# Kernel optimization log

Hardware: AMD Instinct MI355X
Metric: run time of the kernel (lower is better)

The kernel has to match this reference:

```python
import jax, jax.numpy as jnp
import numpy as np

B, T, C = 2, 512, 2048      # batch, seq_len, n_embd (= dim_att)
H, Dh = 32, 64              # num_heads, head_size
D_MIX, D_DECAY = 32, 64     # LoRA ranks (n_embd < 4096)
LAYER_ID, N_LAYER = 12, 24
LN_EPS = 1e-5


def setup_inputs() -> dict:
    key = jax.random.key(0)
    ks = jax.random.split(key, 18)
    s = 1.0 / np.sqrt(C)
    # time_decay init exactly as in the torch module
    ratio_0_to_1 = LAYER_ID / (N_LAYER - 1)
    n = np.arange(C, dtype=np.float64)
    decay_speed = -6.0 + 5.0 * (n / (C - 1)) ** (0.7 + 1.3 * ratio_0_to_1)
    f32 = jnp.float32
    return {
        "x": jax.random.normal(ks[0], (B, T, C), f32),
        # token-shift mix params (stored [C]; torch shape [1,1,C] broadcasts identically)
        "maa_x": jax.random.uniform(ks[1], (C,), f32),
        "maa_r": 0.01 * jax.random.normal(ks[2], (C,), f32),
        "maa_k": 0.01 * jax.random.normal(ks[3], (C,), f32),
        "maa_v": 0.01 * jax.random.normal(ks[4], (C,), f32),
        "maa_w": 0.01 * jax.random.normal(ks[5], (C,), f32),
        "maa_w1": 0.01 * jax.random.normal(ks[6], (C, 4 * D_MIX), f32),
        "maa_w2": 0.01 * jax.random.normal(ks[7], (4, D_MIX, C), f32),
        "time_decay": jnp.asarray(decay_speed, f32),
        "td_w1": 0.01 * jax.random.normal(ks[8], (C, D_DECAY), f32),
        "td_w2": 0.01 * jax.random.normal(ks[9], (D_DECAY, C), f32),
        # projections stored [in, out]; q/k/v have bias, o_proj does not
        "q_w": s * jax.random.normal(ks[10], (C, C), f32),
        "q_b": 0.01 * jax.random.normal(ks[11], (C,), f32),
        "k_w": s * jax.random.normal(ks[12], (C, C), f32),
        "k_b": 0.01 * jax.random.normal(ks[13], (C,), f32),
        "v_w": s * jax.random.normal(ks[14], (C, C), f32),
        "v_b": 0.01 * jax.random.normal(ks[15], (C,), f32),
        "ln_g": jnp.ones((C,), f32),
        "ln_b": jnp.zeros((C,), f32),
        "o_w": s * jax.random.normal(ks[16], (C, C), f32),
    }


def _forward(x, maa_x, maa_r, maa_k, maa_v, maa_w, maa_w1, maa_w2,
             time_decay, td_w1, td_w2, q_w, q_b, k_w, k_b, v_w, v_b,
             ln_g, ln_b, o_w):
    Bz, Tz, Cz = x.shape
    # token shift: dxprev = x_{t-1} - x_t (zero-padded at t=0)
    xprev = jnp.pad(x, ((0, 0), (1, 0), (0, 0)))[:, :Tz]
    dx = xprev - x
    # data-dependent mix coefficients via rank-D_MIX LoRA, 4 heads (r,k,v,w)
    xxx = x + dx * maa_x
    mm = jnp.tanh(xxx @ maa_w1).reshape(Bz, Tz, 4, D_MIX)
    m = jnp.einsum('btrd,rdc->rbtc', mm, maa_w2)  # [4,B,T,C]
    xr = x + dx * (maa_r + m[0])
    xk = x + dx * (maa_k + m[1])
    xv = x + dx * (maa_v + m[2])
    xw = x + dx * (maa_w + m[3])
    q = xr @ q_w + q_b
    k = xk @ k_w + k_b
    v = xv @ v_w + v_b
    # log decay: -exp(time_decay + lora(xw)), clamped to min -5
    w_log = -jnp.exp(time_decay + jnp.tanh(xw @ td_w1) @ td_w2)
    w_log = jnp.maximum(w_log, -5.0)
    k = k * (1.0 - jnp.exp(w_log))
    # split heads, time-major [T,B,H,Dh] for the GLA scan
    def to_tbhd(t):
        return t.reshape(Bz, Tz, H, Dh).transpose(1, 0, 2, 3)
    qh, kh, vh = to_tbhd(q), to_tbhd(k), to_tbhd(v)
    gh = jnp.exp(to_tbhd(w_log))  # per-key-dim decay multiplier in (0,1]
    scale = Dh ** -0.5

    # GLA recurrence: S_t = diag(g_t) S_{t-1} + k_t v_t^T ; o_t = scale * q_t S_t
    def step(S, inp):
        q_t, k_t, v_t, g_t = inp                      # each [B,H,Dh]
        S = S * g_t[..., None] + k_t[..., None] * v_t[..., None, :]
        o_t = jnp.einsum('bhk,bhkv->bhv', q_t, S) * scale
        return S, o_t

    S0 = jnp.zeros((Bz, H, Dh, Dh), x.dtype)
    _, o = jax.lax.scan(step, S0, (qh, kh, vh, gh))   # o: [T,B,H,Dh]
    y = o.transpose(1, 0, 2, 3).reshape(Bz, Tz, Cz)
    # ln_x LayerNorm
    mu = jnp.mean(y, axis=-1, keepdims=True)
    var = jnp.var(y, axis=-1, keepdims=True)
    y = (y - mu) * jax.lax.rsqrt(var + LN_EPS) * ln_g + ln_b
    return y @ o_w


def reference(x, maa_x, maa_r, maa_k, maa_v, maa_w, maa_w1, maa_w2,
              time_decay, td_w1, td_w2, q_w, q_b, k_w, k_b, v_w, v_b,
              ln_g, ln_b, o_w):
    return _forward(x, maa_x, maa_r, maa_k, maa_v, maa_w, maa_w1, maa_w2,
                    time_decay, td_w1, td_w2, q_w, q_b, k_w, k_b, v_w, v_b,
                    ln_g, ln_b, o_w)
```

## Files before the change

kernel.cpp:

```cpp
#include <hip/hip_runtime.h>
#include <hip/hip_bf16.h>
#include <math.h>

#define Bz 2
#define Tz 512
#define Cz 2048
#define Hh 32
#define DH 64
#define NTOK (Bz * Tz)
#define NCH 8
#define NSLICE 32

typedef __hip_bfloat16 bf16;
typedef __attribute__((ext_vector_type(8))) short short8;
typedef __attribute__((ext_vector_type(4))) float f32x4;

__device__ __forceinline__ void load_lds16(const void* g, void* l) {
  __builtin_amdgcn_global_load_lds(
      (const __attribute__((address_space(1))) unsigned int*)g,
      (__attribute__((address_space(3))) unsigned int*)l,
      16, 0, 0);
}

__device__ __forceinline__ f32x4 bf4_to_f32(ushort4 u) {
  f32x4 r;
  r[0] = __builtin_bit_cast(float, (unsigned)u.x << 16);
  r[1] = __builtin_bit_cast(float, (unsigned)u.y << 16);
  r[2] = __builtin_bit_cast(float, (unsigned)u.z << 16);
  r[3] = __builtin_bit_cast(float, (unsigned)u.w << 16);
  return r;
}

template <int MT, int NT>
__device__ __forceinline__ void gemm_core(
    const bf16* __restrict__ A, const bf16* __restrict__ Bt,
    int M0, int N0, int kBeg, int kEnd,
    f32x4 (&acc)[MT / 32][NT / 32]) {
  constexpr int AI = MT / 32, BJ = NT / 32;
  constexpr int TSA = MT / 16, TS = (MT + NT) / 16;
  static_assert(TS % 4 == 0, "strips must divide among 4 waves");
  __shared__ alignas(16) bf16 As[MT * 32];
  __shared__ alignas(16) bf16 Bs[NT * 32];
  int tid = threadIdx.x, lane = tid & 63, wave = tid >> 6;
  int wm = wave & 1, wn = wave >> 1;
  int srow = lane >> 2, scol = (lane & 3) * 8;
  int fr = lane & 15, fk = (lane >> 4) * 8;
  const bf16* rA = As + (wm * (MT / 2) + fr) * 32 + fk;
  const bf16* rB = Bs + (wn * (NT / 2) + fr) * 32 + fk;

  for (int k0 = kBeg; k0 < kEnd; k0 += 32) {
#pragma unroll
    for (int s = wave; s < TS; s += 4) {
      if (s < TSA)
        load_lds16(A + (size_t)(M0 + s * 16 + srow) * Cz + k0 + scol,
                   As + s * 16 * 32);
      else
        load_lds16(Bt + (size_t)(N0 + (s - TSA) * 16 + srow) * Cz + k0 + scol,
                   Bs + (s - TSA) * 16 * 32);
    }
    __syncthreads();
    short8 af[AI], bf[BJ];
#pragma unroll
    for (int i = 0; i < AI; i++) af[i] = *(const short8*)(rA + i * 16 * 32);
#pragma unroll
    for (int j = 0; j < BJ; j++) bf[j] = *(const short8*)(rB + j * 16 * 32);
#pragma unroll
    for (int i = 0; i < AI; i++)
#pragma unroll
      for (int j = 0; j < BJ; j++)
        acc[i][j] = __builtin_amdgcn_mfma_f32_16x16x32_bf16(af[i], bf[j],
                                                            acc[i][j], 0, 0, 0);
    __syncthreads();
  }
}

__global__ __launch_bounds__(256) void k_setup(
    const float* __restrict__ qw, const float* __restrict__ kw,
    const float* __restrict__ vw, const float* __restrict__ ow,
    const float* __restrict__ w1, const float* __restrict__ tdw1,
    const float* __restrict__ w2, const float* __restrict__ tdw2,
    const float* __restrict__ x, const float* __restrict__ maa_x,
    bf16* __restrict__ qwt, bf16* __restrict__ kwt, bf16* __restrict__ vwt,
    bf16* __restrict__ owt, bf16* __restrict__ w1t, bf16* __restrict__ tdw1t,
    bf16* __restrict__ w2t, bf16* __restrict__ tdw2t,
    float* __restrict__ dx, bf16* __restrict__ xxxb) {
  __shared__ float tile[32][33];
  int bid = blockIdx.x;
  int tx = threadIdx.x, ty = threadIdx.y;
  if (bid < 16384) {
    int w = bid >> 12, r = bid & 4095;
    const float* W = w == 0 ? qw : w == 1 ? kw : w == 2 ? vw : ow;
    bf16* O = w == 0 ? qwt : w == 1 ? kwt : w == 2 ? vwt : owt;
    int bx = (r & 63) * 32, by = (r >> 6) * 32;
#pragma unroll
    for (int i = 0; i < 4; i++)
      tile[ty + 8 * i][tx] = W[(size_t)(by + ty + 8 * i) * Cz + bx + tx];
    __syncthreads();
#pragma unroll
    for (int i = 0; i < 4; i++)
      O[(size_t)(bx + ty + 8 * i) * Cz + by + tx] =
          __float2bfloat16(tile[tx][ty + 8 * i]);
  } else if (bid < 16768) {
    int r = bid - 16384;
    int z = r >> 6;
    int bk = (r & 63) * 32;
    const float* W;
    bf16* O;
    int N, bn;
    if (z < 4) { W = w1; O = w1t; N = 128; bn = z * 32; }
    else       { W = tdw1; O = tdw1t; N = 64; bn = (z - 4) * 32; }
#pragma unroll
    for (int i = 0; i < 4; i++)
      tile[ty + 8 * i][tx] = W[(size_t)(bk + ty + 8 * i) * N + bn + tx];
    __syncthreads();
#pragma unroll
    for (int i = 0; i < 4; i++)
      O[(size_t)(bn + ty + 8 * i) * Cz + bk + tx] =
          __float2bfloat16(tile[tx][ty + 8 * i]);
  } else if (bid < 17024) {
    int r2 = bid - 16768;
    int rr = r2 >> 6, c0 = (r2 & 63) * 32;
#pragma unroll
    for (int i = 0; i < 4; i++)
      tile[ty + 8 * i][tx] = w2[(size_t)(rr * 32 + ty + 8 * i) * Cz + c0 + tx];
    __syncthreads();
#pragma unroll
    for (int i = 0; i < 4; i++)
      w2t[(size_t)(rr * 2048 + c0 + ty + 8 * i) * 32 + tx] =
          __float2bfloat16(tile[tx][ty + 8 * i]);
  } else if (bid < 17152) {
    int r2 = bid - 17024;
    int k0 = (r2 & 1) * 32, c0 = (r2 >> 1) * 32;
#pragma unroll
    for (int i = 0; i < 4; i++)
      tile[ty + 8 * i][tx] = tdw2[(size_t)(k0 + ty + 8 * i) * Cz + c0 + tx];
    __syncthreads();
#pragma unroll
    for (int i = 0; i < 4; i++)
      tdw2t[(size_t)(c0 + ty + 8 * i) * 64 + k0 + tx] =
          __float2bfloat16(tile[tx][ty + 8 * i]);
  } else {
    int r = bid - 17152;
    int tid = ty * 32 + tx;
    int i4 = r * 256 + tid;
    int row = i4 >> 9, t = row & (Tz - 1), c4 = i4 & 511;
    const float4* x4 = (const float4*)x;
    float4 xv = x4[i4];
    float4 xp = make_float4(0.f, 0.f, 0.f, 0.f);
    if (t != 0) xp = x4[i4 - 512];
    float4 mx = ((const float4*)maa_x)[c4];
    float4 d, xx;
    d.x = xp.x - xv.x; d.y = xp.y - xv.y; d.z = xp.z - xv.z; d.w = xp.w - xv.w;
    xx.x = xv.x + d.x * mx.x; xx.y = xv.y + d.y * mx.y;
    xx.z = xv.z + d.z * mx.z; xx.w = xv.w + d.w * mx.w;
    ((float4*)dx)[i4] = d;
    ushort4 u;
    u.x = __builtin_bit_cast(unsigned short, __float2bfloat16(xx.x));
    u.y = __builtin_bit_cast(unsigned short, __float2bfloat16(xx.y));
    u.z = __builtin_bit_cast(unsigned short, __float2bfloat16(xx.z));
    u.w = __builtin_bit_cast(unsigned short, __float2bfloat16(xx.w));
    ((ushort4*)xxxb)[i4] = u;
  }
}

template <int NT>
__global__ __launch_bounds__(256) void k_lora_gemm(
    const bf16* __restrict__ A, const bf16* __restrict__ Bt,
    float* __restrict__ part) {
  constexpr int KS = Cz / NSLICE;
  f32x4 acc[4][NT / 32];
#pragma unroll
  for (int i = 0; i < 4; i++)
#pragma unroll
    for (int j = 0; j < NT / 32; j++) acc[i][j] = (f32x4){0.f, 0.f, 0.f, 0.f};
  int bM = blockIdx.x, slice = blockIdx.y;
  gemm_core<128, NT>(A, Bt, bM * 128, 0, slice * KS, slice * KS + KS, acc);
  int lane = threadIdx.x & 63, wave = threadIdx.x >> 6;
  int wm = wave & 1, wn = wave >> 1;
  int r0 = (lane >> 4) * 4, cn = lane & 15;
#pragma unroll
  for (int i = 0; i < 4; i++) {
    int m = bM * 128 + wm * 64 + i * 16 + r0;
#pragma unroll
    for (int j = 0; j < NT / 32; j++) {
      int n = wn * (NT / 2) + j * 16 + cn;
#pragma unroll
      for (int r = 0; r < 4; r++)
        part[((size_t)slice * NTOK + m + r) * NT + n] = acc[i][j][r];
    }
  }
}

__global__ __launch_bounds__(256) void k_reduce_tanh(
    const float* __restrict__ part, bf16* __restrict__ out, int n4) {
  int i = blockIdx.x * 256 + threadIdx.x;
  f32x4 s = (f32x4){0.f, 0.f, 0.f, 0.f};
#pragma unroll 8
  for (int sl = 0; sl < NSLICE; sl++)
    s += *(const f32x4*)&part[(size_t)sl * n4 * 4 + i * 4];
  ushort4 u;
  u.x = __builtin_bit_cast(unsigned short, __float2bfloat16(tanhf(s[0])));
  u.y = __builtin_bit_cast(unsigned short, __float2bfloat16(tanhf(s[1])));
  u.z = __builtin_bit_cast(unsigned short, __float2bfloat16(tanhf(s[2])));
  u.w = __builtin_bit_cast(unsigned short, __float2bfloat16(tanhf(s[3])));
  ((ushort4*)out)[i] = u;
}

__global__ __launch_bounds__(256) void k_mproj_mfma(
    const bf16* __restrict__ mmb, const bf16* __restrict__ w2t,
    const float* __restrict__ x, const float* __restrict__ dx,
    const float* __restrict__ maa_r, const float* __restrict__ maa_k,
    const float* __restrict__ maa_v, const float* __restrict__ maa_w,
    bf16* __restrict__ pxr, bf16* __restrict__ pxk,
    bf16* __restrict__ pxv, bf16* __restrict__ pxw) {
  __shared__ alignas(16) bf16 As[128 * 32];
  __shared__ alignas(16) bf16 Bs[128 * 32];
  int r = blockIdx.z;
  int n0 = blockIdx.x * 128, m0 = blockIdx.y * 128;
  int tid = threadIdx.x, lane = tid & 63, wave = tid >> 6;
  int wm = wave & 1, wn = wave >> 1;
  int srow = lane >> 2, scol = (lane & 3) * 8;
#pragma unroll
  for (int s = wave; s < 16; s += 4) {
    if (s < 8)
      load_lds16(mmb + (size_t)(m0 + s * 16 + srow) * 128 + r * 32 + scol,
                 As + s * 16 * 32);
    else
      load_lds16(w2t + ((size_t)r * 2048 + n0 + (s - 8) * 16 + srow) * 32 + scol,
                 Bs + (s - 8) * 16 * 32);
  }
  __syncthreads();
  int fr = lane & 15, fk = (lane >> 4) * 8;
  const bf16* rA = As + (wm * 64 + fr) * 32 + fk;
  const bf16* rB = Bs + (wn * 64 + fr) * 32 + fk;
  f32x4 acc[4][4];
  short8 af[4], bf[4];
#pragma unroll
  for (int i = 0; i < 4; i++) af[i] = *(const short8*)(rA + i * 16 * 32);
#pragma unroll
  for (int j = 0; j < 4; j++) bf[j] = *(const short8*)(rB + j * 16 * 32);
#pragma unroll
  for (int i = 0; i < 4; i++)
#pragma unroll
    for (int j = 0; j < 4; j++)
      acc[i][j] = __builtin_amdgcn_mfma_f32_16x16x32_bf16(
          af[i], bf[j], (f32x4){0.f, 0.f, 0.f, 0.f}, 0, 0, 0);
  const float* maa = r == 0 ? maa_r : r == 1 ? maa_k : r == 2 ? maa_v : maa_w;
  bf16* dst = r == 0 ? pxr : r == 1 ? pxk : r == 2 ? pxv : pxw;
  int r0 = (lane >> 4) * 4, cn = lane & 15;
#pragma unroll
  for (int i = 0; i < 4; i++) {
    int m = m0 + wm * 64 + i * 16 + r0;
#pragma unroll
    for (int j = 0; j < 4; j++) {
      int n = n0 + wn * 64 + j * 16 + cn;
      float ma = maa[n];
#pragma unroll
      for (int rr = 0; rr < 4; rr++) {
        size_t idx = (size_t)(m + rr) * Cz + n;
        dst[idx] = __float2bfloat16(x[idx] + dx[idx] * (ma + acc[i][j][rr]));
      }
    }
  }
}

__global__ __launch_bounds__(256) void k_tdB_mfma(
    const bf16* __restrict__ twb, const bf16* __restrict__ tdw2t,
    const float* __restrict__ td, float* __restrict__ wlog) {
  __shared__ alignas(16) bf16 As[128 * 32];
  __shared__ alignas(16) bf16 Bs[128 * 32];
  int n0 = blockIdx.x * 128, m0 = blockIdx.y * 128;
  int tid = threadIdx.x, lane = tid & 63, wave = tid >> 6;
  int wm = wave & 1, wn = wave >> 1;
  int srow = lane >> 2, scol = (lane & 3) * 8;
  int fr = lane & 15, fk = (lane >> 4) * 8;
  const bf16* rA = As + (wm * 64 + fr) * 32 + fk;
  const bf16* rB = Bs + (wn * 64 + fr) * 32 + fk;
  f32x4 acc[4][4];
#pragma unroll
  for (int i = 0; i < 4; i++)
#pragma unroll
    for (int j = 0; j < 4; j++) acc[i][j] = (f32x4){0.f, 0.f, 0.f, 0.f};
  for (int k0 = 0; k0 < 64; k0 += 32) {
#pragma unroll
    for (int s = wave; s < 16; s += 4) {
      if (s < 8)
        load_lds16(twb + (size_t)(m0 + s * 16 + srow) * 64 + k0 + scol,
                   As + s * 16 * 32);
      else
        load_lds16(tdw2t + (size_t)(n0 + (s - 8) * 16 + srow) * 64 + k0 + scol,
                   Bs + (s - 8) * 16 * 32);
    }
    __syncthreads();
    short8 af[4], bf[4];
#pragma unroll
    for (int i = 0; i < 4; i++) af[i] = *(const short8*)(rA + i * 16 * 32);
#pragma unroll
    for (int j = 0; j < 4; j++) bf[j] = *(const short8*)(rB + j * 16 * 32);
#pragma unroll
    for (int i = 0; i < 4; i++)
#pragma unroll
      for (int j = 0; j < 4; j++)
        acc[i][j] = __builtin_amdgcn_mfma_f32_16x16x32_bf16(af[i], bf[j],
                                                            acc[i][j], 0, 0, 0);
    __syncthreads();
  }
  int r0 = (lane >> 4) * 4, cn = lane & 15;
#pragma unroll
  for (int i = 0; i < 4; i++) {
    int m = m0 + wm * 64 + i * 16 + r0;
#pragma unroll
    for (int j = 0; j < 4; j++) {
      int n = n0 + wn * 64 + j * 16 + cn;
      float tdc = td[n];
#pragma unroll
      for (int rr = 0; rr < 4; rr++) {
        float wl = -expf(tdc + acc[i][j][rr]);
        wlog[(size_t)(m + rr) * Cz + n] = fmaxf(wl, -5.0f);
      }
    }
  }
}

__global__ __launch_bounds__(256) void k_gemm_qkv_split(
    const bf16* __restrict__ xr, const bf16* __restrict__ xk,
    const bf16* __restrict__ xv, const bf16* __restrict__ qwt,
    const bf16* __restrict__ kwt, const bf16* __restrict__ vwt,
    bf16* __restrict__ part) {
  int z = blockIdx.z, proj = z >> 1, slice = z & 1;
  const bf16* A = proj == 0 ? xr : proj == 1 ? xk : xv;
  const bf16* W = proj == 0 ? qwt : proj == 1 ? kwt : vwt;
  f32x4 acc[4][4];
#pragma unroll
  for (int i = 0; i < 4; i++)
#pragma unroll
    for (int j = 0; j < 4; j++) acc[i][j] = (f32x4){0.f, 0.f, 0.f, 0.f};
  gemm_core<128, 128>(A, W, blockIdx.y * 128, blockIdx.x * 128, slice * 1024,
                      slice * 1024 + 1024, acc);
  int lane = threadIdx.x & 63, wave = threadIdx.x >> 6;
  int wm = wave & 1, wn = wave >> 1;
  int r0 = (lane >> 4) * 4, cn = lane & 15;
  bf16* dst = part + (size_t)z * NTOK * Cz;
#pragma unroll
  for (int i = 0; i < 4; i++) {
    int m = blockIdx.y * 128 + wm * 64 + i * 16 + r0;
#pragma unroll
    for (int j = 0; j < 4; j++) {
      int n = blockIdx.x * 128 + wn * 64 + j * 16 + cn;
#pragma unroll
      for (int r = 0; r < 4; r++)
        dst[(size_t)(m + r) * Cz + n] = __float2bfloat16(acc[i][j][r]);
    }
  }
}

__global__ __launch_bounds__(256) void k_combine_qkv(
    const bf16* __restrict__ part, const float* __restrict__ qb,
    const float* __restrict__ kb, const float* __restrict__ vb,
    float* __restrict__ q, float* __restrict__ k, float* __restrict__ v) {
  int i4 = blockIdx.x * 256 + threadIdx.x;
  int n4 = i4 & 511;
  const size_t P = (size_t)NTOK * Cz;
  const ushort4* pp = (const ushort4*)part;
  const size_t P4 = P / 4;
  float4 b;
  f32x4 s;
  s = bf4_to_f32(pp[i4]) + bf4_to_f32(pp[P4 + i4]);
  b = ((const float4*)qb)[n4];
  s = (s + (f32x4){b.x, b.y, b.z, b.w}) * 0.125f;
  *(f32x4*)&q[(size_t)i4 * 4] = s;
  s = bf4_to_f32(pp[2 * P4 + i4]) + bf4_to_f32(pp[3 * P4 + i4]);
  b = ((const float4*)kb)[n4];
  s = s + (f32x4){b.x, b.y, b.z, b.w};
  *(f32x4*)&k[(size_t)i4 * 4] = s;
  s = bf4_to_f32(pp[4 * P4 + i4]) + bf4_to_f32(pp[5 * P4 + i4]);
  b = ((const float4*)vb)[n4];
  s = s + (f32x4){b.x, b.y, b.z, b.w};
  *(f32x4*)&v[(size_t)i4 * 4] = s;
}

__global__ __launch_bounds__(256) void k_gemm_o_split(
    const bf16* __restrict__ yb, const bf16* __restrict__ owt,
    bf16* __restrict__ part) {
  int z = blockIdx.z;
  f32x4 acc[4][4];
#pragma unroll
  for (int i = 0; i < 4; i++)
#pragma unroll
    for (int j = 0; j < 4; j++) acc[i][j] = (f32x4){0.f, 0.f, 0.f, 0.f};
  gemm_core<128, 128>(yb, owt, blockIdx.y * 128, blockIdx.x * 128, z * 512,
                      z * 512 + 512, acc);
  int lane = threadIdx.x & 63, wave = threadIdx.x >> 6;
  int wm = wave & 1, wn = wave >> 1;
  int r0 = (lane >> 4) * 4, cn = lane & 15;
  bf16* dst = part + (size_t)z * NTOK * Cz;
#pragma unroll
  for (int i = 0; i < 4; i++) {
    int m = blockIdx.y * 128 + wm * 64 + i * 16 + r0;
#pragma unroll
    for (int j = 0; j < 4; j++) {
      int n = blockIdx.x * 128 + wn * 64 + j * 16 + cn;
#pragma unroll
      for (int r = 0; r < 4; r++)
        dst[(size_t)(m + r) * Cz + n] = __float2bfloat16(acc[i][j][r]);
    }
  }
}

__global__ __launch_bounds__(256) void k_combine_o(
    const bf16* __restrict__ part, float* __restrict__ out) {
  int i4 = blockIdx.x * 256 + threadIdx.x;
  const size_t P4 = (size_t)NTOK * Cz / 4;
  const ushort4* pp = (const ushort4*)part;
  f32x4 s = bf4_to_f32(pp[i4]) + bf4_to_f32(pp[P4 + i4]) +
            bf4_to_f32(pp[2 * P4 + i4]) + bf4_to_f32(pp[3 * P4 + i4]);
  *(f32x4*)&out[(size_t)i4 * 4] = s;
}

__global__ __launch_bounds__(256) void k_chunk_prep(
    const float* __restrict__ q, const float* __restrict__ k,
    const float* __restrict__ v, const float* __restrict__ wlog,
    bf16* __restrict__ qt, bf16* __restrict__ kt,
    float* __restrict__ aL, float* __restrict__ U) {
  __shared__ float sCum[64 * 64];
  __shared__ float sKh[64 * 64];
  __shared__ float sV[64 * 64];
  int tid = threadIdx.x;
  int bhc = blockIdx.x;
  int c = bhc & 7, h = (bhc >> 3) & 31, b = bhc >> 8;
  size_t gbase = ((size_t)(b * Tz) + c * 64) * Cz + h * 64;
  size_t cbase = (size_t)bhc * 4096;

#pragma unroll
  for (int i = 0; i < 4; i++) {
    int i4 = tid + i * 256;
    int t = i4 >> 4, dq = i4 & 15;
    size_t g = gbase + (size_t)t * Cz + dq * 4;
    *(float4*)&sCum[t * 64 + dq * 4] = *(const float4*)&wlog[g];
    *(float4*)&sKh[t * 64 + dq * 4] = *(const float4*)&k[g];
    *(float4*)&sV[t * 64 + dq * 4] = *(const float4*)&v[g];
  }
  __syncthreads();
#pragma unroll
  for (int i = 0; i < 16; i++) {
    int idx = tid + i * 256;
    sKh[idx] *= (1.f - expf(sCum[idx]));
  }
  __syncthreads();
  if (tid < 64) {
    float cum = 0.f;
#pragma unroll
    for (int t = 0; t < 64; t++) {
      cum += sCum[t * 64 + tid];
      sCum[t * 64 + tid] = cum;
    }
  }
  __syncthreads();
#pragma unroll
  for (int i = 0; i < 16; i++) {
    int idx = tid + i * 256;
    int t = idx >> 6, d = idx & 63;
    float cl = sCum[t * 64 + d];
    float cL = sCum[63 * 64 + d];
    float kraw = sKh[t * 64 + d];
    float qv = q[gbase + (size_t)t * Cz + d];
    float khv = kraw * expf(cL - cl);
    qt[cbase + idx] = __float2bfloat16(qv * expf(cl));
    kt[cbase + idx] = __float2bfloat16(kraw * expf(-cl));
    sKh[t * 64 + d] = khv;
    if (t == 63) aL[(size_t)bhc * 64 + d] = expf(cl);
  }
  __syncthreads();
  int j = tid & 63, dg = tid >> 6;
  float acc[16];
#pragma unroll
  for (int dd = 0; dd < 16; dd++) acc[dd] = 0.f;
  for (int s = 0; s < 64; s++) {
    float vs = sV[s * 64 + j];
#pragma unroll
    for (int dd = 0; dd < 16; dd++)
      acc[dd] += sKh[s * 64 + dg * 16 + dd] * vs;
  }
#pragma unroll
  for (int dd = 0; dd < 16; dd++)
    U[cbase + (size_t)(dg * 16 + dd) * 64 + j] = acc[dd];
}

__global__ __launch_bounds__(256) void k_chunk_out(
    const bf16* __restrict__ qt, const bf16* __restrict__ kt,
    const float* __restrict__ v, const float* __restrict__ U,
    const float* __restrict__ aL, float* __restrict__ y) {
  __shared__ float sQ[64 * 65];
  __shared__ float sKS[64 * 65];
  __shared__ float sP[64 * 65];
  __shared__ float sV[64 * 64];
  int tid = threadIdx.x;
  int bhc = blockIdx.x;
  int c = bhc & 7, h = (bhc >> 3) & 31, b = bhc >> 8;
  size_t gbase = ((size_t)(b * Tz) + c * 64) * Cz + h * 64;
  size_t cbase = (size_t)bhc * 4096;

#pragma unroll
  for (int i = 0; i < 4; i++) {
    int i4 = tid + i * 256;
    int t = i4 >> 4, dq = i4 & 15;
    ushort4 qu = *(const ushort4*)&qt[cbase + i4 * 4];
    ushort4 ku = *(const ushort4*)&kt[cbase + i4 * 4];
    *(f32x4*)&sQ[t * 65 + dq * 4] = bf4_to_f32(qu);
    *(f32x4*)&sKS[t * 65 + dq * 4] = bf4_to_f32(ku);
  }
  __syncthreads();
  int tg = tid & 15, sg = tid >> 4;
  float p[4][4];
#pragma unroll
  for (int i = 0; i < 4; i++)
#pragma unroll
    for (int jx = 0; jx < 4; jx++) p[i][jx] = 0.f;
  for (int d = 0; d < 64; d++) {
    float qv[4], kv[4];
#pragma unroll
    for (int i = 0; i < 4; i++) qv[i] = sQ[(tg * 4 + i) * 65 + d];
#pragma unroll
    for (int jx = 0; jx < 4; jx++) kv[jx] = sKS[(sg * 4 + jx) * 65 + d];
#pragma unroll
    for (int i = 0; i < 4; i++)
#pragma unroll
      for (int jx = 0; jx < 4; jx++) p[i][jx] += qv[i] * kv[jx];
  }
#pragma unroll
  for (int i = 0; i < 4; i++) {
    int t = tg * 4 + i;
#pragma unroll
    for (int jx = 0; jx < 4; jx++) {
      int s = sg * 4 + jx;
      sP[t * 65 + s] = (s <= t) ? p[i][jx] : 0.f;
    }
  }
  f32x4 Sreg[4];
#pragma unroll
  for (int i = 0; i < 4; i++) Sreg[i] = (f32x4){0.f, 0.f, 0.f, 0.f};
  for (int j = 0; j < c; j++) {
    int bhj = bhc - c + j;
    size_t ub = (size_t)bhj * 4096;
#pragma unroll
    for (int i = 0; i < 4; i++) {
      int i4 = tid + i * 256;
      int d = i4 >> 4;
      float a = aL[(size_t)bhj * 64 + d];
      f32x4 u = *(const f32x4*)&U[ub + (size_t)i4 * 4];
      Sreg[i] = Sreg[i] * a + u;
    }
  }
  __syncthreads();
#pragma unroll
  for (int i = 0; i < 4; i++) {
    int i4 = tid + i * 256;
    int t = i4 >> 4, dq = i4 & 15;
    *(f32x4*)&sKS[t * 64 + dq * 4] = Sreg[i];
    *(float4*)&sV[t * 64 + dq * 4] =
        *(const float4*)&v[gbase + (size_t)t * Cz + dq * 4];
  }
  __syncthreads();
  f32x4 o[4];
#pragma unroll
  for (int i = 0; i < 4; i++) o[i] = (f32x4){0.f, 0.f, 0.f, 0.f};
  for (int s = 0; s < 64; s++) {
    f32x4 vv = *(const f32x4*)&sV[s * 64 + sg * 4];
#pragma unroll
    for (int i = 0; i < 4; i++) {
      float pv = sP[(tg * 4 + i) * 65 + s];
      o[i] += pv * vv;
    }
  }
  for (int d = 0; d < 64; d++) {
    f32x4 sv = *(const f32x4*)&sKS[d * 64 + sg * 4];
#pragma unroll
    for (int i = 0; i < 4; i++) {
      float qv = sQ[(tg * 4 + i) * 65 + d];
      o[i] += qv * sv;
    }
  }
#pragma unroll
  for (int i = 0; i < 4; i++) {
    int t = tg * 4 + i;
    *(f32x4*)&y[gbase + (size_t)t * Cz + sg * 4] = o[i];
  }
}

__global__ __launch_bounds__(256) void k_ln(
    const float* __restrict__ y, const float* __restrict__ lg,
    const float* __restrict__ lb, bf16* __restrict__ yb) {
  __shared__ float red[8];
  int t = blockIdx.x;
  int tid = threadIdx.x;
  const float4* y4 = (const float4*)(y + (size_t)t * Cz);
  float4 vals[2];
  float s = 0.f, s2 = 0.f;
#pragma unroll
  for (int u = 0; u < 2; u++) {
    float4 a = y4[tid + 256 * u];
    vals[u] = a;
    s += a.x + a.y + a.z + a.w;
    s2 += a.x * a.x + a.y * a.y + a.z * a.z + a.w * a.w;
  }
#pragma unroll
  for (int off = 32; off > 0; off >>= 1) {
    s += __shfl_down(s, off);
    s2 += __shfl_down(s2, off);
  }
  if ((tid & 63) == 0) {
    red[(tid >> 6) * 2] = s;
    red[(tid >> 6) * 2 + 1] = s2;
  }
  __syncthreads();
  float ts = red[0] + red[2] + red[4] + red[6];
  float ts2 = red[1] + red[3] + red[5] + red[7];
  float mu = ts / (float)Cz;
  float var = ts2 / (float)Cz - mu * mu;
  float inv = rsqrtf(var + 1e-5f);
  bf16* outp = yb + (size_t)t * Cz;
#pragma unroll
  for (int u = 0; u < 2; u++) {
    int c0 = (tid + 256 * u) * 4;
    float4 a = vals[u];
    outp[c0 + 0] = __float2bfloat16((a.x - mu) * inv * lg[c0 + 0] + lb[c0 + 0]);
    outp[c0 + 1] = __float2bfloat16((a.y - mu) * inv * lg[c0 + 1] + lb[c0 + 1]);
    outp[c0 + 2] = __float2bfloat16((a.z - mu) * inv * lg[c0 + 2] + lb[c0 + 2]);
    outp[c0 + 3] = __float2bfloat16((a.w - mu) * inv * lg[c0 + 3] + lb[c0 + 3]);
  }
}

extern "C" void kernel_launch(void* const* d_in, const int* in_sizes, int n_in,
                              void* d_out, int out_size, void* d_ws,
                              size_t ws_size, hipStream_t stream) {
  const float* x      = (const float*)d_in[0];
  const float* maa_x  = (const float*)d_in[1];
  const float* maa_r  = (const float*)d_in[2];
  const float* maa_k  = (const float*)d_in[3];
  const float* maa_v  = (const float*)d_in[4];
  const float* maa_w  = (const float*)d_in[5];
  const float* maa_w1 = (const float*)d_in[6];
  const float* maa_w2 = (const float*)d_in[7];
  const float* tdcay  = (const float*)d_in[8];
  const float* td_w1  = (const float*)d_in[9];
  const float* td_w2  = (const float*)d_in[10];
  const float* q_w    = (const float*)d_in[11];
  const float* q_b    = (const float*)d_in[12];
  const float* k_w    = (const float*)d_in[13];
  const float* k_b    = (const float*)d_in[14];
  const float* v_w    = (const float*)d_in[15];
  const float* v_b    = (const float*)d_in[16];
  const float* ln_g   = (const float*)d_in[17];
  const float* ln_b   = (const float*)d_in[18];
  const float* o_w    = (const float*)d_in[19];
  float* out = (float*)d_out;

  char* p = (char*)d_ws;
  auto alloc = [&](size_t bytes) {
    char* r = p;
    p += (bytes + 255) & ~(size_t)255;
    return r;
  };
  const size_t WB = (size_t)Cz * Cz * sizeof(bf16);
  const size_t AF = (size_t)NTOK * Cz * sizeof(float);
  const size_t AB = (size_t)NTOK * Cz * sizeof(bf16);

  bf16* qwt = (bf16*)alloc(WB);
  bf16* kwt = (bf16*)alloc(WB);
  bf16* vwt = (bf16*)alloc(WB);
  bf16* owt = (bf16*)alloc(WB);
  char* xslot = (char*)alloc(AF);
  char* mmslot = (char*)alloc((size_t)NTOK * 128 * sizeof(float));
  bf16* xr = (bf16*)alloc(AB);
  bf16* xk = (bf16*)alloc(AB);
  bf16* xv = (bf16*)alloc(AB);
  char* xwslot = (char*)alloc(AF);
  bf16* twb = (bf16*)alloc((size_t)NTOK * 64 * sizeof(bf16));
  float* wlog = (float*)alloc(AF);
  char* scratch24 = (char*)alloc(3 * AF);
  char* qkvf = (char*)alloc(3 * AF);
  bf16* yb = (bf16*)alloc(AB);

  bf16* xxxb = (bf16*)xslot;
  bf16* w1t = (bf16*)(xslot + 4 * 1024 * 1024);
  bf16* tdw1t = (bf16*)(xslot + 4 * 1024 * 1024 + 512 * 1024);
  bf16* w2t = (bf16*)(xslot + 4 * 1024 * 1024 + 768 * 1024);
  bf16* tdw2t = (bf16*)(xslot + 4 * 1024 * 1024 + 1280 * 1024);
  bf16* qt = (bf16*)xslot;
  bf16* kt = (bf16*)(xslot + 4 * 1024 * 1024);
  bf16* xwb = (bf16*)xwslot;
  float* U = (float*)xwslot;
  bf16* mmb = (bf16*)mmslot;
  float* aLbuf = (float*)(mmslot + 256 * 1024);

  float* dx = (float*)qkvf;
  float* q = (float*)qkvf;
  float* k = (float*)(qkvf + AF);
  float* v = (float*)(qkvf + 2 * AF);

  float* mm_part = (float*)scratch24;
  float* tw_part = (float*)(scratch24 + 2 * AF);
  bf16* qkv_part = (bf16*)scratch24;
  float* y = (float*)scratch24;
  bf16* o_part = (bf16*)scratch24;

  k_setup<<<19200, dim3(32, 8), 0, stream>>>(
      q_w, k_w, v_w, o_w, maa_w1, td_w1, maa_w2, td_w2, x, maa_x, qwt, kwt,
      vwt, owt, w1t, tdw1t, w2t, tdw2t, dx, xxxb);
  k_lora_gemm<128><<<dim3(8, NSLICE), 256, 0, stream>>>(xxxb, w1t, mm_part);
  k_reduce_tanh<<<128, 256, 0, stream>>>(mm_part, mmb, NTOK * 128 / 4);
  k_mproj_mfma<<<dim3(16, 8, 4), 256, 0, stream>>>(
      mmb, w2t, x, dx, maa_r, maa_k, maa_v, maa_w, xr, xk, xv, xwb);
  k_lora_gemm<64><<<dim3(8, NSLICE), 256, 0, stream>>>(xwb, tdw1t, tw_part);
  k_reduce_tanh<<<64, 256, 0, stream>>>(tw_part, twb, NTOK * 64 / 4);
  k_tdB_mfma<<<dim3(16, 8), 256, 0, stream>>>(twb, tdw2t, tdcay, wlog);
  k_gemm_qkv_split<<<dim3(16, 8, 6), 256, 0, stream>>>(xr, xk, xv, qwt, kwt,
                                                       vwt, qkv_part);
  k_combine_qkv<<<2048, 256, 0, stream>>>(qkv_part, q_b, k_b, v_b, q, k, v);
  k_chunk_prep<<<512, 256, 0, stream>>>(q, k, v, wlog, qt, kt, aLbuf, U);
  k_chunk_out<<<512, 256, 0, stream>>>(qt, kt, v, U, aLbuf, y);
  k_ln<<<NTOK, 256, 0, stream>>>(y, ln_g, ln_b, yb);
  k_gemm_o_split<<<dim3(16, 8, 4), 256, 0, stream>>>(yb, owt, o_part);
  k_combine_o<<<2048, 256, 0, stream>>>(o_part, out);
}
```

Before: 292.5 us.

## Fuse decay LoRA into QKV GEMM launch and fold QKV combine into chunk kernels

The decay-LoRA down-projection (with its tanh) now runs as 8 extra blocks inside the QKV split-K GEMM launch, without K-splitting. This removes a separate GEMM and reduce launch. The QKV combine kernel is gone: chunk_prep and chunk_out read the bf16 split-K partials directly and add the bias, so no fp32 q/k/v round trip through memory. In exchange, those 8 LoRA blocks each walk the full K=2048 and may become stragglers. V partials are also read twice, once per chunk kernel.

```diff
diff --git a/kernel.cpp b/kernel.cpp
--- a/kernel.cpp
+++ b/kernel.cpp
@@ -31,16 +31,24 @@
   return r;
 }
 
+__device__ __forceinline__ ushort4 f32_to_bf4(f32x4 s) {
+  ushort4 u;
+  u.x = __builtin_bit_cast(unsigned short, __float2bfloat16(s[0]));
+  u.y = __builtin_bit_cast(unsigned short, __float2bfloat16(s[1]));
+  u.z = __builtin_bit_cast(unsigned short, __float2bfloat16(s[2]));
+  u.w = __builtin_bit_cast(unsigned short, __float2bfloat16(s[3]));
+  return u;
+}
+
 template <int MT, int NT>
 __device__ __forceinline__ void gemm_core(
+    bf16* As, bf16* Bs,
     const bf16* __restrict__ A, const bf16* __restrict__ Bt,
     int M0, int N0, int kBeg, int kEnd,
     f32x4 (&acc)[MT / 32][NT / 32]) {
   constexpr int AI = MT / 32, BJ = NT / 32;
   constexpr int TSA = MT / 16, TS = (MT + NT) / 16;
   static_assert(TS % 4 == 0, "strips must divide among 4 waves");
-  __shared__ alignas(16) bf16 As[MT * 32];
-  __shared__ alignas(16) bf16 Bs[NT * 32];
   int tid = threadIdx.x, lane = tid & 63, wave = tid >> 6;
   int wm = wave & 1, wn = wave >> 1;
   int srow = lane >> 2, scol = (lane & 3) * 8;
@@ -154,27 +162,23 @@
     xx.x = xv.x + d.x * mx.x; xx.y = xv.y + d.y * mx.y;
     xx.z = xv.z + d.z * mx.z; xx.w = xv.w + d.w * mx.w;
     ((float4*)dx)[i4] = d;
-    ushort4 u;
-    u.x = __builtin_bit_cast(unsigned short, __float2bfloat16(xx.x));
-    u.y = __builtin_bit_cast(unsigned short, __float2bfloat16(xx.y));
-    u.z = __builtin_bit_cast(unsigned short, __float2bfloat16(xx.z));
-    u.w = __builtin_bit_cast(unsigned short, __float2bfloat16(xx.w));
-    ((ushort4*)xxxb)[i4] = u;
-  }
-}
-
-template <int NT>
-__global__ __launch_bounds__(256) void k_lora_gemm(
+    ((ushort4*)xxxb)[i4] = f32_to_bf4((f32x4){xx.x, xx.y, xx.z, xx.w});
+  }
+}
+
+__global__ __launch_bounds__(256) void k_lora_gemm128(
     const bf16* __restrict__ A, const bf16* __restrict__ Bt,
     float* __restrict__ part) {
+  __shared__ alignas(16) bf16 smem[256 * 32];
   constexpr int KS = Cz / NSLICE;
-  f32x4 acc[4][NT / 32];
+  f32x4 acc[4][4];
 #pragma unroll
   for (int i = 0; i < 4; i++)
 #pragma unroll
-    for (int j = 0; j < NT / 32; j++) acc[i][j] = (f32x4){0.f, 0.f, 0.f, 0.f};
+    for (int j = 0; j < 4; j++) acc[i][j] = (f32x4){0.f, 0.f, 0.f, 0.f};
   int bM = blockIdx.x, slice = blockIdx.y;
-  gemm_core<128, NT>(A, Bt, bM * 128, 0, slice * KS, slice * KS + KS, acc);
+  gemm_core<128, 128>(smem, smem + 128 * 32, A, Bt, bM * 128, 0, slice * KS,
+                      slice * KS + KS, acc);
   int lane = threadIdx.x & 63, wave = threadIdx.x >> 6;
   int wm = wave & 1, wn = wave >> 1;
   int r0 = (lane >> 4) * 4, cn = lane & 15;
@@ -182,11 +186,11 @@
   for (int i = 0; i < 4; i++) {
     int m = bM * 128 + wm * 64 + i * 16 + r0;
 #pragma unroll
-    for (int j = 0; j < NT / 32; j++) {
-      int n = wn * (NT / 2) + j * 16 + cn;
+    for (int j = 0; j < 4; j++) {
+      int n = wn * 64 + j * 16 + cn;
 #pragma unroll
       for (int r = 0; r < 4; r++)
-        part[((size_t)slice * NTOK + m + r) * NT + n] = acc[i][j][r];
+        part[((size_t)slice * NTOK + m + r) * 128 + n] = acc[i][j][r];
     }
   }
 }
@@ -198,12 +202,8 @@
 #pragma unroll 8
   for (int sl = 0; sl < NSLICE; sl++)
     s += *(const f32x4*)&part[(size_t)sl * n4 * 4 + i * 4];
-  ushort4 u;
-  u.x = __builtin_bit_cast(unsigned short, __float2bfloat16(tanhf(s[0])));
-  u.y = __builtin_bit_cast(unsigned short, __float2bfloat16(tanhf(s[1])));
-  u.z = __builtin_bit_cast(unsigned short, __float2bfloat16(tanhf(s[2])));
-  u.w = __builtin_bit_cast(unsigned short, __float2bfloat16(tanhf(s[3])));
-  ((ushort4*)out)[i] = u;
+  f32x4 o = {tanhf(s[0]), tanhf(s[1]), tanhf(s[2]), tanhf(s[3])};
+  ((ushort4*)out)[i] = f32_to_bf4(o);
 }
 
 __global__ __launch_bounds__(256) void k_mproj_mfma(
@@ -264,6 +264,66 @@
   }
 }
 
+__global__ __launch_bounds__(256) void k_qkv_lora(
+    const bf16* __restrict__ xr, const bf16* __restrict__ xk,
+    const bf16* __restrict__ xv, const bf16* __restrict__ qwt,
+    const bf16* __restrict__ kwt, const bf16* __restrict__ vwt,
+    bf16* __restrict__ part, const bf16* __restrict__ xwb,
+    const bf16* __restrict__ tdw1t, bf16* __restrict__ twb) {
+  __shared__ alignas(16) bf16 smem[256 * 32];
+  int bid = blockIdx.x;
+  int lane = threadIdx.x & 63, wave = threadIdx.x >> 6;
+  int wm = wave & 1, wn = wave >> 1;
+  int r0 = (lane >> 4) * 4, cn = lane & 15;
+  if (bid < 8) {
+    f32x4 acc[4][2];
+#pragma unroll
+    for (int i = 0; i < 4; i++)
+#pragma unroll
+      for (int j = 0; j < 2; j++) acc[i][j] = (f32x4){0.f, 0.f, 0.f, 0.f};
+    gemm_core<128, 64>(smem, smem + 128 * 32, xwb, tdw1t, bid * 128, 0, 0, Cz,
+                       acc);
+#pragma unroll
+    for (int i = 0; i < 4; i++) {
+      int m = bid * 128 + wm * 64 + i * 16 + r0;
+#pragma unroll
+      for (int j = 0; j < 2; j++) {
+        int n = wn * 32 + j * 16 + cn;
+#pragma unroll
+        for (int r = 0; r < 4; r++)
+          twb[(size_t)(m + r) * 64 + n] =
+              __float2bfloat16(tanhf(acc[i][j][r]));
+      }
+    }
+  } else {
+    int r = bid - 8;
+    int z = r >> 7, xy = r & 127;
+    int nx = xy & 15, my = xy >> 4;
+    int proj = z >> 1, slice = z & 1;
+    const bf16* A = proj == 0 ? xr : proj == 1 ? xk : xv;
+    const bf16* W = proj == 0 ? qwt : proj == 1 ? kwt : vwt;
+    f32x4 acc[4][4];
+#pragma unroll
+    for (int i = 0; i < 4; i++)
+#pragma unroll
+      for (int j = 0; j < 4; j++) acc[i][j] = (f32x4){0.f, 0.f, 0.f, 0.f};
+    gemm_core<128, 128>(smem, smem + 128 * 32, A, W, my * 128, nx * 128,
+                        slice * 1024, slice * 1024 + 1024, acc);
+    bf16* dst = part + (size_t)z * NTOK * Cz;
+#pragma unroll
+    for (int i = 0; i < 4; i++) {
+      int m = my * 128 + wm * 64 + i * 16 + r0;
+#pragma unroll
+      for (int j = 0; j < 4; j++) {
+        int n = nx * 128 + wn * 64 + j * 16 + cn;
+#pragma unroll
+        for (int rr = 0; rr < 4; rr++)
+          dst[(size_t)(m + rr) * Cz + n] = __float2bfloat16(acc[i][j][rr]);
+      }
+    }
+  }
+}
+
 __global__ __launch_bounds__(256) void k_tdB_mfma(
     const bf16* __restrict__ twb, const bf16* __restrict__ tdw2t,
     const float* __restrict__ td, float* __restrict__ wlog) {
@@ -322,106 +382,11 @@
   }
 }
 
-__global__ __launch_bounds__(256) void k_gemm_qkv_split(
-    const bf16* __restrict__ xr, const bf16* __restrict__ xk,
-    const bf16* __restrict__ xv, const bf16* __restrict__ qwt,
-    const bf16* __restrict__ kwt, const bf16* __restrict__ vwt,
-    bf16* __restrict__ part) {
-  int z = blockIdx.z, proj = z >> 1, slice = z & 1;
-  const bf16* A = proj == 0 ? xr : proj == 1 ? xk : xv;
-  const bf16* W = proj == 0 ? qwt : proj == 1 ? kwt : vwt;
-  f32x4 acc[4][4];
-#pragma unroll
-  for (int i = 0; i < 4; i++)
-#pragma unroll
-    for (int j = 0; j < 4; j++) acc[i][j] = (f32x4){0.f, 0.f, 0.f, 0.f};
-  gemm_core<128, 128>(A, W, blockIdx.y * 128, blockIdx.x * 128, slice * 1024,
-                      slice * 1024 + 1024, acc);
-  int lane = threadIdx.x & 63, wave = threadIdx.x >> 6;
-  int wm = wave & 1, wn = wave >> 1;
-  int r0 = (lane >> 4) * 4, cn = lane & 15;
-  bf16* dst = part + (size_t)z * NTOK * Cz;
-#pragma unroll
-  for (int i = 0; i < 4; i++) {
-    int m = blockIdx.y * 128 + wm * 64 + i * 16 + r0;
-#pragma unroll
-    for (int j = 0; j < 4; j++) {
-      int n = blockIdx.x * 128 + wn * 64 + j * 16 + cn;
-#pragma unroll
-      for (int r = 0; r < 4; r++)
-        dst[(size_t)(m + r) * Cz + n] = __float2bfloat16(acc[i][j][r]);
-    }
-  }
-}
-
-__global__ __launch_bounds__(256) void k_combine_qkv(
+__global__ __launch_bounds__(256) void k_chunk_prep(
     const bf16* __restrict__ part, const float* __restrict__ qb,
     const float* __restrict__ kb, const float* __restrict__ vb,
-    float* __restrict__ q, float* __restrict__ k, float* __restrict__ v) {
-  int i4 = blockIdx.x * 256 + threadIdx.x;
-  int n4 = i4 & 511;
-  const size_t P = (size_t)NTOK * Cz;
-  const ushort4* pp = (const ushort4*)part;
-  const size_t P4 = P / 4;
-  float4 b;
-  f32x4 s;
-  s = bf4_to_f32(pp[i4]) + bf4_to_f32(pp[P4 + i4]);
-  b = ((const float4*)qb)[n4];
-  s = (s + (f32x4){b.x, b.y, b.z, b.w}) * 0.125f;
-  *(f32x4*)&q[(size_t)i4 * 4] = s;
-  s = bf4_to_f32(pp[2 * P4 + i4]) + bf4_to_f32(pp[3 * P4 + i4]);
-  b = ((const float4*)kb)[n4];
-  s = s + (f32x4){b.x, b.y, b.z, b.w};
-  *(f32x4*)&k[(size_t)i4 * 4] = s;
-  s = bf4_to_f32(pp[4 * P4 + i4]) + bf4_to_f32(pp[5 * P4 + i4]);
-  b = ((const float4*)vb)[n4];
-  s = s + (f32x4){b.x, b.y, b.z, b.w};
-  *(f32x4*)&v[(size_t)i4 * 4] = s;
-}
-
-__global__ __launch_bounds__(256) void k_gemm_o_split(
-    const bf16* __restrict__ yb, const bf16* __restrict__ owt,
-    bf16* __restrict__ part) {
-  int z = blockIdx.z;
-  f32x4 acc[4][4];
-#pragma unroll
-  for (int i = 0; i < 4; i++)
-#pragma unroll
-    for (int j = 0; j < 4; j++) acc[i][j] = (f32x4){0.f, 0.f, 0.f, 0.f};
-  gemm_core<128, 128>(yb, owt, blockIdx.y * 128, blockIdx.x * 128, z * 512,
-                      z * 512 + 512, acc);
-  int lane = threadIdx.x & 63, wave = threadIdx.x >> 6;
-  int wm = wave & 1, wn = wave >> 1;
-  int r0 = (lane >> 4) * 4, cn = lane & 15;
-  bf16* dst = part + (size_t)z * NTOK * Cz;
-#pragma unroll
-  for (int i = 0; i < 4; i++) {
-    int m = blockIdx.y * 128 + wm * 64 + i * 16 + r0;
-#pragma unroll
-    for (int j = 0; j < 4; j++) {
-      int n = blockIdx.x * 128 + wn * 64 + j * 16 + cn;
-#pragma unroll
-      for (int r = 0; r < 4; r++)
-        dst[(size_t)(m + r) * Cz + n] = __float2bfloat16(acc[i][j][r]);
-    }
-  }
-}
-
-__global__ __launch_bounds__(256) void k_combine_o(
-    const bf16* __restrict__ part, float* __restrict__ out) {
-  int i4 = blockIdx.x * 256 + threadIdx.x;
-  const size_t P4 = (size_t)NTOK * Cz / 4;
-  const ushort4* pp = (const ushort4*)part;
-  f32x4 s = bf4_to_f32(pp[i4]) + bf4_to_f32(pp[P4 + i4]) +
-            bf4_to_f32(pp[2 * P4 + i4]) + bf4_to_f32(pp[3 * P4 + i4]);
-  *(f32x4*)&out[(size_t)i4 * 4] = s;
-}
-
-__global__ __launch_bounds__(256) void k_chunk_prep(
-    const float* __restrict__ q, const float* __restrict__ k,
-    const float* __restrict__ v, const float* __restrict__ wlog,
-    bf16* __restrict__ qt, bf16* __restrict__ kt,
-    float* __restrict__ aL, float* __restrict__ U) {
+    const float* __restrict__ wlog, bf16* __restrict__ qt,
+    bf16* __restrict__ kt, float* __restrict__ aL, float* __restrict__ U) {
   __shared__ float sCum[64 * 64];
   __shared__ float sKh[64 * 64];
   __shared__ float sV[64 * 64];
@@ -430,15 +395,24 @@
   int c = bhc & 7, h = (bhc >> 3) & 31, b = bhc >> 8;
   size_t gbase = ((size_t)(b * Tz) + c * 64) * Cz + h * 64;
   size_t cbase = (size_t)bhc * 4096;
+  const ushort4* pp = (const ushort4*)part;
+  const size_t P4 = (size_t)NTOK * Cz / 4;
 
 #pragma unroll
   for (int i = 0; i < 4; i++) {
     int i4 = tid + i * 256;
     int t = i4 >> 4, dq = i4 & 15;
-    size_t g = gbase + (size_t)t * Cz + dq * 4;
-    *(float4*)&sCum[t * 64 + dq * 4] = *(const float4*)&wlog[g];
-    *(float4*)&sKh[t * 64 + dq * 4] = *(const float4*)&k[g];
-    *(float4*)&sV[t * 64 + dq * 4] = *(const float4*)&v[g];
+    size_t ge = gbase + (size_t)t * Cz + dq * 4;
+    size_t gq = ge / 4;
+    float4 kb4 = ((const float4*)kb)[h * 16 + dq];
+    float4 vb4 = ((const float4*)vb)[h * 16 + dq];
+    f32x4 kvv = bf4_to_f32(pp[2 * P4 + gq]) + bf4_to_f32(pp[3 * P4 + gq]) +
+                (f32x4){kb4.x, kb4.y, kb4.z, kb4.w};
+    f32x4 vvv = bf4_to_f32(pp[4 * P4 + gq]) + bf4_to_f32(pp[5 * P4 + gq]) +
+                (f32x4){vb4.x, vb4.y, vb4.z, vb4.w};
+    *(float4*)&sCum[t * 64 + dq * 4] = *(const float4*)&wlog[ge];
+    *(f32x4*)&sKh[t * 64 + dq * 4] = kvv;
+    *(f32x4*)&sV[t * 64 + dq * 4] = vvv;
   }
   __syncthreads();
 #pragma unroll
@@ -457,18 +431,32 @@
   }
   __syncthreads();
 #pragma unroll
-  for (int i = 0; i < 16; i++) {
-    int idx = tid + i * 256;
-    int t = idx >> 6, d = idx & 63;
-    float cl = sCum[t * 64 + d];
-    float cL = sCum[63 * 64 + d];
-    float kraw = sKh[t * 64 + d];
-    float qv = q[gbase + (size_t)t * Cz + d];
-    float khv = kraw * expf(cL - cl);
-    qt[cbase + idx] = __float2bfloat16(qv * expf(cl));
-    kt[cbase + idx] = __float2bfloat16(kraw * expf(-cl));
-    sKh[t * 64 + d] = khv;
-    if (t == 63) aL[(size_t)bhc * 64 + d] = expf(cl);
+  for (int i = 0; i < 4; i++) {
+    int i4 = tid + i * 256;
+    int t = i4 >> 4, dq = i4 & 15;
+    size_t ge = gbase + (size_t)t * Cz + dq * 4;
+    size_t gq = ge / 4;
+    float4 qb4 = ((const float4*)qb)[h * 16 + dq];
+    f32x4 qv = (bf4_to_f32(pp[gq]) + bf4_to_f32(pp[P4 + gq]) +
+                (f32x4){qb4.x, qb4.y, qb4.z, qb4.w}) * 0.125f;
+    f32x4 cl = *(const f32x4*)&sCum[t * 64 + dq * 4];
+    f32x4 cL = *(const f32x4*)&sCum[63 * 64 + dq * 4];
+    f32x4 kraw = *(const f32x4*)&sKh[t * 64 + dq * 4];
+    f32x4 qtv, ktv, khv;
+#pragma unroll
+    for (int e = 0; e < 4; e++) {
+      qtv[e] = qv[e] * expf(cl[e]);
+      ktv[e] = kraw[e] * expf(-cl[e]);
+      khv[e] = kraw[e] * expf(cL[e] - cl[e]);
+    }
+    ((ushort4*)qt)[cbase / 4 + i4] = f32_to_bf4(qtv);
+    ((ushort4*)kt)[cbase / 4 + i4] = f32_to_bf4(ktv);
+    *(f32x4*)&sKh[t * 64 + dq * 4] = khv;
+    if (t == 63) {
+#pragma unroll
+      for (int e = 0; e < 4; e++)
+        aL[(size_t)bhc * 64 + dq * 4 + e] = expf(cl[e]);
+    }
   }
   __syncthreads();
   int j = tid & 63, dg = tid >> 6;
@@ -488,8 +476,9 @@
 
 __global__ __launch_bounds__(256) void k_chunk_out(
     const bf16* __restrict__ qt, const bf16* __restrict__ kt,
-    const float* __restrict__ v, const float* __restrict__ U,
-    const float* __restrict__ aL, float* __restrict__ y) {
+    const bf16* __restrict__ part, const float* __restrict__ vb,
+    const float* __restrict__ U, const float* __restrict__ aL,
+    float* __restrict__ y) {
   __shared__ float sQ[64 * 65];
   __shared__ float sKS[64 * 65];
   __shared__ float sP[64 * 65];
@@ -499,6 +488,8 @@
   int c = bhc & 7, h = (bhc >> 3) & 31, b = bhc >> 8;
   size_t gbase = ((size_t)(b * Tz) + c * 64) * Cz + h * 64;
   size_t cbase = (size_t)bhc * 4096;
+  const ushort4* pp = (const ushort4*)part;
+  const size_t P4 = (size_t)NTOK * Cz / 4;
 
 #pragma unroll
   for (int i = 0; i < 4; i++) {
@@ -508,6 +499,11 @@
     ushort4 ku = *(const ushort4*)&kt[cbase + i4 * 4];
     *(f32x4*)&sQ[t * 65 + dq * 4] = bf4_to_f32(qu);
     *(f32x4*)&sKS[t * 65 + dq * 4] = bf4_to_f32(ku);
+    size_t gq = (gbase + (size_t)t * Cz + dq * 4) / 4;
+    float4 vb4 = ((const float4*)vb)[h * 16 + dq];
+    f32x4 vvv = bf4_to_f32(pp[4 * P4 + gq]) + bf4_to_f32(pp[5 * P4 + gq]) +
+                (f32x4){vb4.x, vb4.y, vb4.z, vb4.w};
+    *(f32x4*)&sV[t * 64 + dq * 4] = vvv;
   }
   __syncthreads();
   int tg = tid & 15, sg = tid >> 4;
@@ -557,8 +553,6 @@
     int i4 = tid + i * 256;
     int t = i4 >> 4, dq = i4 & 15;
     *(f32x4*)&sKS[t * 64 + dq * 4] = Sreg[i];
-    *(float4*)&sV[t * 64 + dq * 4] =
-        *(const float4*)&v[gbase + (size_t)t * Cz + dq * 4];
   }
   __syncthreads();
   f32x4 o[4];
@@ -628,6 +622,45 @@
     outp[c0 + 2] = __float2bfloat16((a.z - mu) * inv * lg[c0 + 2] + lb[c0 + 2]);
     outp[c0 + 3] = __float2bfloat16((a.w - mu) * inv * lg[c0 + 3] + lb[c0 + 3]);
   }
+}
+
+__global__ __launch_bounds__(256) void k_gemm_o_split(
+    const bf16* __restrict__ yb, const bf16* __restrict__ owt,
+    bf16* __restrict__ part) {
+  __shared__ alignas(16) bf16 smem[256 * 32];
+  int z = blockIdx.z;
+  f32x4 acc[4][4];
+#pragma unroll
+  for (int i = 0; i < 4; i++)
+#pragma unroll
+    for (int j = 0; j < 4; j++) acc[i][j] = (f32x4){0.f, 0.f, 0.f, 0.f};
+  gemm_core<128, 128>(smem, smem + 128 * 32, yb, owt, blockIdx.y * 128,
+                      blockIdx.x * 128, z * 512, z * 512 + 512, acc);
+  int lane = threadIdx.x & 63, wave = threadIdx.x >> 6;
+  int wm = wave & 1, wn = wave >> 1;
+  int r0 = (lane >> 4) * 4, cn = lane & 15;
+  bf16* dst = part + (size_t)z * NTOK * Cz;
+#pragma unroll
+  for (int i = 0; i < 4; i++) {
+    int m = blockIdx.y * 128 + wm * 64 + i * 16 + r0;
+#pragma unroll
+    for (int j = 0; j < 4; j++) {
+      int n = blockIdx.x * 128 + wn * 64 + j * 16 + cn;
+#pragma unroll
+      for (int r = 0; r < 4; r++)
+        dst[(size_t)(m + r) * Cz + n] = __float2bfloat16(acc[i][j][r]);
+    }
+  }
+}
+
+__global__ __launch_bounds__(256) void k_combine_o(
+    const bf16* __restrict__ part, float* __restrict__ out) {
+  int i4 = blockIdx.x * 256 + threadIdx.x;
+  const size_t P4 = (size_t)NTOK * Cz / 4;
+  const ushort4* pp = (const ushort4*)part;
+  f32x4 s = bf4_to_f32(pp[i4]) + bf4_to_f32(pp[P4 + i4]) +
+            bf4_to_f32(pp[2 * P4 + i4]) + bf4_to_f32(pp[3 * P4 + i4]);
+  *(f32x4*)&out[(size_t)i4 * 4] = s;
 }
 
 extern "C" void kernel_launch(void* const* d_in, const int* in_sizes, int n_in,
@@ -678,7 +711,7 @@
   bf16* twb = (bf16*)alloc((size_t)NTOK * 64 * sizeof(bf16));
   float* wlog = (float*)alloc(AF);
   char* scratch24 = (char*)alloc(3 * AF);
-  char* qkvf = (char*)alloc(3 * AF);
+  float* dx = (float*)alloc(AF);
   bf16* yb = (bf16*)alloc(AB);
 
   bf16* xxxb = (bf16*)xslot;
@@ -693,13 +726,7 @@
   bf16* mmb = (bf16*)mmslot;
   float* aLbuf = (float*)(mmslot + 256 * 1024);
 
-  float* dx = (float*)qkvf;
-  float* q = (float*)qkvf;
-  float* k = (float*)(qkvf + AF);
-  float* v = (float*)(qkvf + 2 * AF);
-
   float* mm_part = (float*)scratch24;
-  float* tw_part = (float*)(scratch24 + 2 * AF);
   bf16* qkv_part = (bf16*)scratch24;
   float* y = (float*)scratch24;
   bf16* o_part = (bf16*)scratch24;
@@ -707,18 +734,16 @@
   k_setup<<<19200, dim3(32, 8), 0, stream>>>(
       q_w, k_w, v_w, o_w, maa_w1, td_w1, maa_w2, td_w2, x, maa_x, qwt, kwt,
       vwt, owt, w1t, tdw1t, w2t, tdw2t, dx, xxxb);
-  k_lora_gemm<128><<<dim3(8, NSLICE), 256, 0, stream>>>(xxxb, w1t, mm_part);
+  k_lora_gemm128<<<dim3(8, NSLICE), 256, 0, stream>>>(xxxb, w1t, mm_part);
   k_reduce_tanh<<<128, 256, 0, stream>>>(mm_part, mmb, NTOK * 128 / 4);
   k_mproj_mfma<<<dim3(16, 8, 4), 256, 0, stream>>>(
       mmb, w2t, x, dx, maa_r, maa_k, maa_v, maa_w, xr, xk, xv, xwb);
-  k_lora_gemm<64><<<dim3(8, NSLICE), 256, 0, stream>>>(xwb, tdw1t, tw_part);
-  k_reduce_tanh<<<64, 256, 0, stream>>>(tw_part, twb, NTOK * 64 / 4);
+  k_qkv_lora<<<776, 256, 0, stream>>>(xr, xk, xv, qwt, kwt, vwt, qkv_part,
+                                      xwb, tdw1t, twb);
   k_tdB_mfma<<<dim3(16, 8), 256, 0, stream>>>(twb, tdw2t, tdcay, wlog);
-  k_gemm_qkv_split<<<dim3(16, 8, 6), 256, 0, stream>>>(xr, xk, xv, qwt, kwt,
-                                                       vwt, qkv_part);
-  k_combine_qkv<<<2048, 256, 0, stream>>>(qkv_part, q_b, k_b, v_b, q, k, v);
-  k_chunk_prep<<<512, 256, 0, stream>>>(q, k, v, wlog, qt, kt, aLbuf, U);
-  k_chunk_out<<<512, 256, 0, stream>>>(qt, kt, v, U, aLbuf, y);
+  k_chunk_prep<<<512, 256, 0, stream>>>(qkv_part, q_b, k_b, v_b, wlog, qt, kt,
+                                        aLbuf, U);
+  k_chunk_out<<<512, 256, 0, stream>>>(qt, kt, qkv_part, v_b, U, aLbuf, y);
   k_ln<<<NTOK, 256, 0, stream>>>(y, ln_g, ln_b, yb);
   k_gemm_o_split<<<dim3(16, 8, 4), 256, 0, stream>>>(yb, owt, o_part);
   k_combine_o<<<2048, 256, 0, stream>>>(o_part, out);
```

After: 292.6 us. Within noise of the previous version (+0.0%).
